# Kernel tuning notes

Hardware: AMD Instinct MI355X
Metric: run time of the kernel (lower is better)

The kernel has to match this reference:

```python
import jax, jax.numpy as jnp
import numpy as np

T = 1_000_000      # number of feature rows
D = 82             # STSIM feature dim (hardcoded Linear(82, 1))
NUM_GROUPS = 256   # N = mask.max() + 1 in the original (fixed for jit)


def setup_inputs() -> dict:
    key = jax.random.key(0)
    k1, k2, k3, k4, k5 = jax.random.split(key, 5)
    X1 = jax.random.normal(k1, (T, D), jnp.float32)
    X2 = jax.random.normal(k2, (T, D), jnp.float32)
    Y = jax.random.normal(k3, (T,), jnp.float32)
    mask = jax.random.randint(k4, (T,), 0, NUM_GROUPS)
    # Linear(82,1,bias=False) weight; positive (matches init_weight = 1/var)
    # so sqrt(M((X1-X2)^2)) is real.
    W = jax.random.uniform(k5, (1, D), jnp.float32, 0.01, 1.0)
    return {"X1": X1, "X2": X2, "Y": Y, "W": W, "mask": mask}


def _criterion(x, Y, mask):
    # Vectorized version of the per-group Pearson-correlation loop:
    # one pass of segment reductions instead of N full-array boolean masks.
    seg = lambda v: jax.ops.segment_sum(v, mask, num_segments=NUM_GROUPS)
    counts = seg(jnp.ones_like(x))                      # [N]
    xc = x - (seg(x) / counts)[mask]                    # per-group centered
    yc = Y - (seg(Y) / counts)[mask]
    nom = seg(xc * yc)                                  # [N]
    denom = jnp.sqrt(seg(xc * xc) * seg(yc * yc))       # [N]
    return jnp.sum(jnp.abs(nom / denom)) / NUM_GROUPS


def reference(X1, X2, Y, W, mask):
    # pred = sqrt(Linear((X1 - X2)^2))  -> [T, 1]
    pred = jnp.sqrt(((X1 - X2) ** 2) @ W.T)
    coeff = _criterion(pred[:, 0], Y, mask)
    return coeff, pred
```

## Files before the change

kernel.cpp:

```cpp
#include <hip/hip_runtime.h>
#include <hip/hip_bf16.h>

#define T_ROWS 1000000
#define D 82
#define NG 256

#define WS_CNT   0
#define WS_SUMP  256
#define WS_SUMY  512
#define WS_MEANP 768
#define WS_MEANY 1024
#define WS_SXY   1280
#define WS_SXX   1536
#define WS_SYY   1792
#define WS_FLOATS 2048

__global__ __launch_bounds__(256) void pred_kernel(
    const float* __restrict__ X1, const float* __restrict__ X2,
    const float* __restrict__ Y, const float* __restrict__ W,
    const int* __restrict__ mask, float* __restrict__ pred_out,
    float* __restrict__ ws)
{
    __shared__ float lds_w[D];
    __shared__ float lds_cnt[NG], lds_sp[NG], lds_sy[NG];
    const int t = threadIdx.x;
    if (t < D) lds_w[t] = W[t];
    lds_cnt[t] = 0.f; lds_sp[t] = 0.f; lds_sy[t] = 0.f;
    __syncthreads();

    const int pair = blockIdx.x * 256 + t;
    if (pair < T_ROWS / 2) {
        const float4* __restrict__ p1 = (const float4*)(X1 + (size_t)pair * (2 * D));
        const float4* __restrict__ p2 = (const float4*)(X2 + (size_t)pair * (2 * D));
        float accA = 0.f, accB = 0.f;
        #pragma unroll 5
        for (int k = 0; k < 20; ++k) {
            float4 a = p1[k], b = p2[k];
            float d;
            d = a.x - b.x; accA += d * d * lds_w[4 * k + 0];
            d = a.y - b.y; accA += d * d * lds_w[4 * k + 1];
            d = a.z - b.z; accA += d * d * lds_w[4 * k + 2];
            d = a.w - b.w; accA += d * d * lds_w[4 * k + 3];
        }
        {
            float4 a = p1[20], b = p2[20];
            float d;
            d = a.x - b.x; accA += d * d * lds_w[80];
            d = a.y - b.y; accA += d * d * lds_w[81];
            d = a.z - b.z; accB += d * d * lds_w[0];
            d = a.w - b.w; accB += d * d * lds_w[1];
        }
        #pragma unroll 5
        for (int k = 21; k < 41; ++k) {
            float4 a = p1[k], b = p2[k];
            const int c = 4 * k - 82;
            float d;
            d = a.x - b.x; accB += d * d * lds_w[c + 0];
            d = a.y - b.y; accB += d * d * lds_w[c + 1];
            d = a.z - b.z; accB += d * d * lds_w[c + 2];
            d = a.w - b.w; accB += d * d * lds_w[c + 3];
        }
        const float pA = sqrtf(accA);
        const float pB = sqrtf(accB);
        pred_out[2 * pair]     = pA;
        pred_out[2 * pair + 1] = pB;

        const int2   gg = *(const int2*)(mask + 2 * (size_t)pair);
        const float2 yy = *(const float2*)(Y + 2 * (size_t)pair);
        atomicAdd(&lds_cnt[gg.x], 1.f);  atomicAdd(&lds_cnt[gg.y], 1.f);
        atomicAdd(&lds_sp[gg.x], pA);    atomicAdd(&lds_sp[gg.y], pB);
        atomicAdd(&lds_sy[gg.x], yy.x);  atomicAdd(&lds_sy[gg.y], yy.y);
    }
    __syncthreads();
    atomicAdd(&ws[WS_CNT  + t], lds_cnt[t]);
    atomicAdd(&ws[WS_SUMP + t], lds_sp[t]);
    atomicAdd(&ws[WS_SUMY + t], lds_sy[t]);
}

__global__ void means_kernel(float* __restrict__ ws)
{
    const int g = threadIdx.x;
    const float c = ws[WS_CNT + g];
    ws[WS_MEANP + g] = ws[WS_SUMP + g] / c;
    ws[WS_MEANY + g] = ws[WS_SUMY + g] / c;
}

__global__ __launch_bounds__(256) void corr_kernel(
    const float* __restrict__ pred, const float* __restrict__ Y,
    const int* __restrict__ mask, float* __restrict__ ws)
{
    __shared__ float mP[NG], mY[NG], sxy[NG], sxx[NG], syy[NG];
    const int t = threadIdx.x;
    mP[t] = ws[WS_MEANP + t];
    mY[t] = ws[WS_MEANY + t];
    sxy[t] = 0.f; sxx[t] = 0.f; syy[t] = 0.f;
    __syncthreads();

    const int stride = gridDim.x * blockDim.x;
    for (int r = blockIdx.x * blockDim.x + t; r < T_ROWS; r += stride) {
        const int g = mask[r];
        const float xc = pred[r] - mP[g];
        const float yc = Y[r]    - mY[g];
        atomicAdd(&sxy[g], xc * yc);
        atomicAdd(&sxx[g], xc * xc);
        atomicAdd(&syy[g], yc * yc);
    }
    __syncthreads();
    atomicAdd(&ws[WS_SXY + t], sxy[t]);
    atomicAdd(&ws[WS_SXX + t], sxx[t]);
    atomicAdd(&ws[WS_SYY + t], syy[t]);
}

__global__ void final_kernel(const float* __restrict__ ws, float* __restrict__ out)
{
    __shared__ float red[NG];
    const int g = threadIdx.x;
    const float r = ws[WS_SXY + g] / sqrtf(ws[WS_SXX + g] * ws[WS_SYY + g]);
    red[g] = fabsf(r);
    __syncthreads();
    for (int s = 128; s > 0; s >>= 1) {
        if (g < s) red[g] += red[g + s];
        __syncthreads();
    }
    if (g == 0) out[0] = red[0] / (float)NG;
}

extern "C" void kernel_launch(void* const* d_in, const int* in_sizes, int n_in,
                              void* d_out, int out_size, void* d_ws, size_t ws_size,
                              hipStream_t stream)
{
    const float* X1   = (const float*)d_in[0];
    const float* X2   = (const float*)d_in[1];
    const float* Y    = (const float*)d_in[2];
    const float* W    = (const float*)d_in[3];
    const int*   mask = (const int*)d_in[4];
    float* out = (float*)d_out;
    float* ws  = (float*)d_ws;

    hipMemsetAsync(ws, 0, WS_FLOATS * sizeof(float), stream);

    const int pairs = T_ROWS / 2;
    const int gridA = (pairs + 255) / 256;
    pred_kernel<<<gridA, 256, 0, stream>>>(X1, X2, Y, W, mask, out + 1, ws);
    means_kernel<<<1, 256, 0, stream>>>(ws);
    corr_kernel<<<1024, 256, 0, stream>>>(out + 1, Y, mask, ws);
    final_kernel<<<1, 256, 0, stream>>>(ws, out);
}
```

Measured before the change: 726.6 us.

## Fuse prediction and correlation into one pass using raw-moment sums and async LDS staging

```diff
diff --git a/kernel.cpp b/kernel.cpp
--- a/kernel.cpp
+++ b/kernel.cpp
@@ -1,122 +1,153 @@
 #include <hip/hip_runtime.h>
-#include <hip/hip_bf16.h>
 
-#define T_ROWS 1000000
-#define D 82
-#define NG 256
+#define T_ROWS   1000000
+#define D        82
+#define NG       256
+#define RPC      64
+#define CHB      20992
+#define NCHUNKS  15625
+#define NBLOCKS  256
 
-#define WS_CNT   0
-#define WS_SUMP  256
-#define WS_SUMY  512
-#define WS_MEANP 768
-#define WS_MEANY 1024
-#define WS_SXY   1280
-#define WS_SXX   1536
-#define WS_SYY   1792
-#define WS_FLOATS 2048
+#define WSD_CNT 0
+#define WSD_SP  256
+#define WSD_SPP 512
+#define WSD_SY  768
+#define WSD_SYY 1024
+#define WSD_SPY 1280
 
-__global__ __launch_bounds__(256) void pred_kernel(
+typedef const __attribute__((address_space(1))) unsigned int* gp1_t;
+typedef __attribute__((address_space(3))) unsigned int* lp3_t;
+
+__device__ __forceinline__ void gl16(const void* g, const void* l) {
+    __builtin_amdgcn_global_load_lds((gp1_t)(unsigned long long)g,
+                                     (lp3_t)(unsigned int)(unsigned long long)l,
+                                     16, 0, 0);
+}
+
+__global__ __launch_bounds__(256) void fused_kernel(
     const float* __restrict__ X1, const float* __restrict__ X2,
-    const float* __restrict__ Y, const float* __restrict__ W,
+    const float* __restrict__ Y,  const float* __restrict__ W,
     const int* __restrict__ mask, float* __restrict__ pred_out,
-    float* __restrict__ ws)
+    double* __restrict__ wsd)
 {
-    __shared__ float lds_w[D];
-    __shared__ float lds_cnt[NG], lds_sp[NG], lds_sy[NG];
-    const int t = threadIdx.x;
-    if (t < D) lds_w[t] = W[t];
-    lds_cnt[t] = 0.f; lds_sp[t] = 0.f; lds_sy[t] = 0.f;
+    __shared__ __align__(16) float sbuf[3][10496];
+    __shared__ float t_cnt[NG], t_sp[NG], t_spp[NG], t_sy[NG], t_syy[NG], t_spy[NG];
+
+    const int tid  = threadIdx.x;
+    const int wid  = tid >> 6;
+    const int lane = tid & 63;
+    const int b    = blockIdx.x;
+
+    t_cnt[tid] = 0.f; t_sp[tid]  = 0.f; t_spp[tid] = 0.f;
+    t_sy[tid]  = 0.f; t_syy[tid] = 0.f; t_spy[tid] = 0.f;
+
+    const int rloc = tid >> 2;
+    const int q    = tid & 3;
+    const int e0   = q * 20;
+    float wreg[20];
+    #pragma unroll
+    for (int k = 0; k < 20; ++k) wreg[k] = W[e0 + k];
+    float w20 = 0.f, w21 = 0.f;
+    if (q == 3) { w20 = W[80]; w21 = W[81]; }
+
     __syncthreads();
 
-    const int pair = blockIdx.x * 256 + t;
-    if (pair < T_ROWS / 2) {
-        const float4* __restrict__ p1 = (const float4*)(X1 + (size_t)pair * (2 * D));
-        const float4* __restrict__ p2 = (const float4*)(X2 + (size_t)pair * (2 * D));
-        float accA = 0.f, accB = 0.f;
-        #pragma unroll 5
-        for (int k = 0; k < 20; ++k) {
-            float4 a = p1[k], b = p2[k];
-            float d;
-            d = a.x - b.x; accA += d * d * lds_w[4 * k + 0];
-            d = a.y - b.y; accA += d * d * lds_w[4 * k + 1];
-            d = a.z - b.z; accA += d * d * lds_w[4 * k + 2];
-            d = a.w - b.w; accA += d * d * lds_w[4 * k + 3];
+    const int nJ = (NCHUNKS - b + 255) >> 8;
+
+    auto stage = [&](int c, int bi) {
+        const char* g1 = (const char*)X1 + (size_t)c * CHB;
+        const char* g2 = (const char*)X2 + (size_t)c * CHB;
+        char* l = (char*)&sbuf[bi][0];
+        for (int s = wid; s < 21; s += 4) {
+            if (s < 20) {
+                gl16(g1 + s * 1024 + lane * 16, l + s * 1024);
+                gl16(g2 + s * 1024 + lane * 16, l + CHB + s * 1024);
+            } else if (lane < 32) {
+                gl16(g1 + 20480 + lane * 16, l + 20480);
+                gl16(g2 + 20480 + lane * 16, l + CHB + 20480);
+            }
         }
-        {
-            float4 a = p1[20], b = p2[20];
-            float d;
-            d = a.x - b.x; accA += d * d * lds_w[80];
-            d = a.y - b.y; accA += d * d * lds_w[81];
-            d = a.z - b.z; accB += d * d * lds_w[0];
-            d = a.w - b.w; accB += d * d * lds_w[1];
+    };
+
+    int   mnext = 0; float ynext = 0.f;
+    if (q == 0) { const int r0 = b * RPC + rloc; mnext = mask[r0]; ynext = Y[r0]; }
+
+    stage(b, 0);
+    stage(b + 256, 1);
+
+    for (int j = 0; j < nJ; ++j) {
+        const int c  = b + (j << 8);
+        const int bi = j % 3;
+
+        if (j == nJ - 1) asm volatile("s_waitcnt vmcnt(0)" ::: "memory");
+        else             asm volatile("s_waitcnt vmcnt(10)" ::: "memory");
+        __builtin_amdgcn_s_barrier();
+        asm volatile("" ::: "memory");
+
+        if (j + 2 < nJ) stage(b + ((j + 2) << 8), (j + 2) % 3);
+
+        const int   mcur = mnext; const float ycur = ynext;
+        if (q == 0 && j + 1 < nJ) {
+            const int rn = (c + 256) * RPC + rloc;
+            mnext = mask[rn]; ynext = Y[rn];
         }
-        #pragma unroll 5
-        for (int k = 21; k < 41; ++k) {
-            float4 a = p1[k], b = p2[k];
-            const int c = 4 * k - 82;
-            float d;
-            d = a.x - b.x; accB += d * d * lds_w[c + 0];
-            d = a.y - b.y; accB += d * d * lds_w[c + 1];
-            d = a.z - b.z; accB += d * d * lds_w[c + 2];
-            d = a.w - b.w; accB += d * d * lds_w[c + 3];
+
+        const float* row1 = &sbuf[bi][rloc * 82];
+        const float* row2 = row1 + 5248;
+        float acc = 0.f;
+        #pragma unroll
+        for (int k = 0; k < 20; k += 2) {
+            const float2 a  = *(const float2*)(row1 + e0 + k);
+            const float2 bb = *(const float2*)(row2 + e0 + k);
+            const float d0 = a.x - bb.x, d1 = a.y - bb.y;
+            acc += d0 * d0 * wreg[k];
+            acc += d1 * d1 * wreg[k + 1];
         }
-        const float pA = sqrtf(accA);
-        const float pB = sqrtf(accB);
-        pred_out[2 * pair]     = pA;
-        pred_out[2 * pair + 1] = pB;
+        if (q == 3) {
+            const float2 a  = *(const float2*)(row1 + 80);
+            const float2 bb = *(const float2*)(row2 + 80);
+            const float d0 = a.x - bb.x, d1 = a.y - bb.y;
+            acc += d0 * d0 * w20 + d1 * d1 * w21;
+        }
+        acc += __shfl_xor(acc, 1);
+        acc += __shfl_xor(acc, 2);
 
-        const int2   gg = *(const int2*)(mask + 2 * (size_t)pair);
-        const float2 yy = *(const float2*)(Y + 2 * (size_t)pair);
-        atomicAdd(&lds_cnt[gg.x], 1.f);  atomicAdd(&lds_cnt[gg.y], 1.f);
-        atomicAdd(&lds_sp[gg.x], pA);    atomicAdd(&lds_sp[gg.y], pB);
-        atomicAdd(&lds_sy[gg.x], yy.x);  atomicAdd(&lds_sy[gg.y], yy.y);
+        if (q == 0) {
+            const float p = sqrtf(acc);
+            pred_out[c * RPC + rloc] = p;
+            const int g = mcur;
+            atomicAdd(&t_cnt[g], 1.f);
+            atomicAdd(&t_sp [g], p);
+            atomicAdd(&t_spp[g], p * p);
+            atomicAdd(&t_sy [g], ycur);
+            atomicAdd(&t_syy[g], ycur * ycur);
+            atomicAdd(&t_spy[g], p * ycur);
+        }
     }
+
     __syncthreads();
-    atomicAdd(&ws[WS_CNT  + t], lds_cnt[t]);
-    atomicAdd(&ws[WS_SUMP + t], lds_sp[t]);
-    atomicAdd(&ws[WS_SUMY + t], lds_sy[t]);
+    atomicAdd(&wsd[WSD_CNT + tid], (double)t_cnt[tid]);
+    atomicAdd(&wsd[WSD_SP  + tid], (double)t_sp [tid]);
+    atomicAdd(&wsd[WSD_SPP + tid], (double)t_spp[tid]);
+    atomicAdd(&wsd[WSD_SY  + tid], (double)t_sy [tid]);
+    atomicAdd(&wsd[WSD_SYY + tid], (double)t_syy[tid]);
+    atomicAdd(&wsd[WSD_SPY + tid], (double)t_spy[tid]);
 }
 
-__global__ void means_kernel(float* __restrict__ ws)
-{
-    const int g = threadIdx.x;
-    const float c = ws[WS_CNT + g];
-    ws[WS_MEANP + g] = ws[WS_SUMP + g] / c;
-    ws[WS_MEANY + g] = ws[WS_SUMY + g] / c;
-}
-
-__global__ __launch_bounds__(256) void corr_kernel(
-    const float* __restrict__ pred, const float* __restrict__ Y,
-    const int* __restrict__ mask, float* __restrict__ ws)
-{
-    __shared__ float mP[NG], mY[NG], sxy[NG], sxx[NG], syy[NG];
-    const int t = threadIdx.x;
-    mP[t] = ws[WS_MEANP + t];
-    mY[t] = ws[WS_MEANY + t];
-    sxy[t] = 0.f; sxx[t] = 0.f; syy[t] = 0.f;
-    __syncthreads();
-
-    const int stride = gridDim.x * blockDim.x;
-    for (int r = blockIdx.x * blockDim.x + t; r < T_ROWS; r += stride) {
-        const int g = mask[r];
-        const float xc = pred[r] - mP[g];
-        const float yc = Y[r]    - mY[g];
-        atomicAdd(&sxy[g], xc * yc);
-        atomicAdd(&sxx[g], xc * xc);
-        atomicAdd(&syy[g], yc * yc);
-    }
-    __syncthreads();
-    atomicAdd(&ws[WS_SXY + t], sxy[t]);
-    atomicAdd(&ws[WS_SXX + t], sxx[t]);
-    atomicAdd(&ws[WS_SYY + t], syy[t]);
-}
-
-__global__ void final_kernel(const float* __restrict__ ws, float* __restrict__ out)
+__global__ void final_kernel(const double* __restrict__ wsd, float* __restrict__ out)
 {
     __shared__ float red[NG];
     const int g = threadIdx.x;
-    const float r = ws[WS_SXY + g] / sqrtf(ws[WS_SXX + g] * ws[WS_SYY + g]);
-    red[g] = fabsf(r);
+    const double n   = wsd[WSD_CNT + g];
+    const double sp  = wsd[WSD_SP  + g];
+    const double spp = wsd[WSD_SPP + g];
+    const double sy  = wsd[WSD_SY  + g];
+    const double syy = wsd[WSD_SYY + g];
+    const double spy = wsd[WSD_SPY + g];
+    const double sxy = spy - sp * sy / n;
+    const double sxx = spp - sp * sp / n;
+    const double syc = syy - sy * sy / n;
+    red[g] = (float)fabs(sxy / sqrt(sxx * syc));
     __syncthreads();
     for (int s = 128; s > 0; s >>= 1) {
         if (g < s) red[g] += red[g + s];
@@ -135,14 +166,8 @@
     const float* W    = (const float*)d_in[3];
     const int*   mask = (const int*)d_in[4];
     float* out = (float*)d_out;
-    float* ws  = (float*)d_ws;
 
-    hipMemsetAsync(ws, 0, WS_FLOATS * sizeof(float), stream);
-
-    const int pairs = T_ROWS / 2;
-    const int gridA = (pairs + 255) / 256;
-    pred_kernel<<<gridA, 256, 0, stream>>>(X1, X2, Y, W, mask, out + 1, ws);
-    means_kernel<<<1, 256, 0, stream>>>(ws);
-    corr_kernel<<<1024, 256, 0, stream>>>(out + 1, Y, mask, ws);
-    final_kernel<<<1, 256, 0, stream>>>(ws, out);
+    hipMemsetAsync(d_ws, 0, 6 * NG * sizeof(double), stream);
+    fused_kernel<<<NBLOCKS, 256, 0, stream>>>(X1, X2, Y, W, mask, out + 1, (double*)d_ws);
+    final_kernel<<<1, NG, 0, stream>>>((const double*)d_ws, out);
 }
```

After: 642.2 us. -11.6%, faster.
